# Kernel optimization log

Measured on AMD Instinct MI355X. Metric: run time of the kernel, lower is better.

## Reference

```python
import jax, jax.numpy as jnp
import numpy as np

DIM = 192
HEADS = 6
HD = DIM // HEADS            # 32
RES = (32, 64, 64)           # D, H, W
WS = (4, 4, 4)               # window size
NW_TOK = WS[0] * WS[1] * WS[2]   # 64 tokens per window
L = RES[0] * RES[1] * RES[2]     # 131072
HIDDEN = 4 * DIM
B = 2


def _rel_pos_index():
    # faithful to the torch buffer construction (3D branch)
    coords = np.stack(np.meshgrid(*[np.arange(w) for w in WS], indexing='ij'))  # (3, wd, wh, ww)
    cf = coords.reshape(3, -1)                     # (3, 64)
    rel = cf[:, :, None] - cf[:, None, :]          # (3, 64, 64)
    rel = rel.transpose(1, 2, 0).astype(np.int64)  # (64, 64, 3)
    for i in range(3):
        rel[:, :, i] += WS[i] - 1
    rel[:, :, 0] *= (2 * WS[1] - 1) * (2 * WS[2] - 1)
    rel[:, :, 1] *= 2 * WS[2] - 1
    return rel.sum(-1)                             # (64, 64)


def setup_inputs() -> dict:
    key = jax.random.key(0)
    ks = jax.random.split(key, 8)
    s = 0.02
    d = {}
    d['skip'] = jax.random.normal(ks[0], (B, L, DIM), jnp.float32)
    d['x_up'] = jax.random.normal(ks[1], (B, L, DIM), jnp.float32)
    # norms
    d['g1'] = jnp.ones((DIM,), jnp.float32); d['be1'] = jnp.zeros((DIM,), jnp.float32)
    d['g2'] = jnp.ones((DIM,), jnp.float32); d['be2'] = jnp.zeros((DIM,), jnp.float32)
    # attention params
    d['Wkv'] = jax.random.normal(ks[2], (DIM, 2 * DIM), jnp.float32) * s
    d['bkv'] = jnp.zeros((2 * DIM,), jnp.float32)
    d['Wproj'] = jax.random.normal(ks[3], (DIM, DIM), jnp.float32) * s
    d['bproj'] = jnp.zeros((DIM,), jnp.float32)
    d['bias_table'] = jax.random.normal(ks[4], ((2 * WS[0] - 1) * (2 * WS[1] - 1) * (2 * WS[2] - 1), HEADS), jnp.float32) * s
    d['rel_idx'] = jnp.asarray(_rel_pos_index(), jnp.int32)
    # MLP params
    d['W1'] = jax.random.normal(ks[5], (DIM, HIDDEN), jnp.float32) * s
    d['b1'] = jnp.zeros((HIDDEN,), jnp.float32)
    d['W2'] = jax.random.normal(ks[6], (HIDDEN, DIM), jnp.float32) * s
    d['b2'] = jnp.zeros((DIM,), jnp.float32)
    return d


def _ln(x, g, b):
    mu = x.mean(-1, keepdims=True)
    var = x.var(-1, keepdims=True)
    return (x - mu) * jax.lax.rsqrt(var + 1e-5) * g + b


def _win_part(x):
    # x: (B, D, H, W, C) -> (B*nW, 64, C)
    D, H, W = RES; wd, wh, ww = WS
    x = x.reshape(B, D // wd, wd, H // wh, wh, W // ww, ww, DIM)
    x = x.transpose(0, 1, 3, 5, 2, 4, 6, 7)
    return x.reshape(-1, NW_TOK, DIM)


def _win_rev(w):
    # (B*nW, 64, C) -> (B, L, C)
    D, H, W = RES; wd, wh, ww = WS
    x = w.reshape(B, D // wd, H // wh, W // ww, wd, wh, ww, DIM)
    x = x.transpose(0, 1, 4, 2, 5, 3, 6, 7)
    return x.reshape(B, L, DIM)


def reference(skip, x_up, g1, be1, g2, be2, Wkv, bkv, Wproj, bproj,
              bias_table, rel_idx, W1, b1, W2, b2):
    shortcut = skip
    s = _ln(skip, g1, be1).reshape(B, *RES, DIM)
    u = _ln(x_up, g1, be1).reshape(B, *RES, DIM)
    sw = _win_part(s)   # kv source: (Bw, 64, C)
    uw = _win_part(u)   # q source
    Bw = sw.shape[0]
    kv = (sw @ Wkv + bkv).reshape(Bw, NW_TOK, 2, HEADS, HD)
    k = kv[:, :, 0].transpose(0, 2, 1, 3)   # (Bw, h, 64, hd)
    v = kv[:, :, 1].transpose(0, 2, 1, 3)
    q = uw.reshape(Bw, NW_TOK, HEADS, HD).transpose(0, 2, 1, 3)
    scale = HD ** -0.5
    attn = jnp.einsum('bhqd,bhkd->bhqk', q * scale, k)
    bias = bias_table[rel_idx.reshape(-1)].reshape(NW_TOK, NW_TOK, HEADS).transpose(2, 0, 1)
    attn = jax.nn.softmax(attn + bias[None], axis=-1)
    o = jnp.einsum('bhqk,bhkd->bhqd', attn, v).transpose(0, 2, 1, 3).reshape(Bw, NW_TOK, DIM)
    o = o @ Wproj + bproj
    x = shortcut + _win_rev(o)
    h = _ln(x, g2, be2)
    h = jax.nn.gelu(h @ W1 + b1, approximate=False)
    return x + (h @ W2 + b2)
```

## Files before the change

kernel.cpp:

```cpp
#include <hip/hip_runtime.h>
#include <hip/hip_bf16.h>

typedef __hip_bfloat16 bf16;
typedef short s8v __attribute__((ext_vector_type(8)));
typedef float f32x4 __attribute__((ext_vector_type(4)));

__device__ __forceinline__ float b2f(bf16 v) { return __bfloat162float(v); }
__device__ __forceinline__ bf16 f2b(float v) { return __float2bfloat16(v); }

union H8 { bf16 h[8]; s8v v; uint2 u2[2]; };

__device__ __forceinline__ float gelu_f(float v) {
    float z = fabsf(v) * 0.70710678118654752f;
    float t = 1.f / (1.f + 0.3275911f * z);
    float poly = t * (0.254829592f + t * (-0.284496736f + t * (1.421413741f +
                 t * (-1.453152027f + t * 1.061405429f))));
    float erfz = 1.f - poly * __expf(-z * z);
    erfz = copysignf(erfz, v);
    return 0.5f * v * (1.f + erfz);
}

__device__ __forceinline__ void stage_frag(const bf16* __restrict__ img, bf16* lds,
                                           int nseg, int wv, int lane) {
    for (int seg = wv; seg < nseg; seg += 4) {
        __builtin_amdgcn_global_load_lds(
            (const __attribute__((address_space(1))) void*)(img + seg * 512 + (lane << 3)),
            (__attribute__((address_space(3))) void*)(lds + seg * 512),
            16, 0, 0);
    }
}

__global__ __launch_bounds__(256) void k_prep(
    const float* __restrict__ Wkv, const float* __restrict__ Wproj,
    const float* __restrict__ W1,  const float* __restrict__ W2,
    bf16* __restrict__ ws)
{
    int t = blockIdx.x * 256 + threadIdx.x;
    if (t >= 50688) return;
    int k, n, ld;
    const float* W;
    bf16* dst;
    if (t < 9216) {
        int c = t / 1152, r = t % 1152;
        int tile = r >> 6, lane = r & 63;
        int ks = tile / 3, nt = tile % 3;
        n = c * 48 + nt * 16 + (lane & 15);
        k = ks * 32 + (lane >> 4) * 8;
        W = Wkv; ld = 384; dst = ws + t * 8;
    } else if (t < 13824) {
        int t2 = t - 9216;
        int c = t2 / 1152, r = t2 % 1152;
        int tile = r >> 6, lane = r & 63;
        int ks = tile / 3, nt = tile % 3;
        n = c * 48 + nt * 16 + (lane & 15);
        k = ks * 32 + (lane >> 4) * 8;
        W = Wproj; ld = 192; dst = ws + 73728 + t2 * 8;
    } else {
        int t3 = t - 13824;
        int c = t3 / 1536, r = t3 % 1536;
        int half = r / 768, rr = r % 768;
        int tile = rr >> 6, lane = rr & 63;
        int lr = lane & 15, g = lane >> 4;
        if (half == 0) {
            int ks = tile >> 1, nt2 = tile & 1;
            n = c * 32 + nt2 * 16 + lr; k = ks * 32 + g * 8; W = W1; ld = 768;
        } else {
            n = tile * 16 + lr; k = c * 32 + g * 8; W = W2; ld = 192;
        }
        dst = ws + 110592 + t3 * 8;
    }
    #pragma unroll
    for (int e = 0; e < 8; ++e) dst[e] = f2b(W[(k + e) * ld + n]);
}

__global__ __launch_bounds__(256, 2) void k_attn(
    const float* __restrict__ skip, const float* __restrict__ xup,
    const float* __restrict__ g1,   const float* __restrict__ be1,
    const bf16*  __restrict__ imgKv,const float* __restrict__ bkv,
    const bf16*  __restrict__ imgPr,const float* __restrict__ bproj,
    const float* __restrict__ btab, const int*  __restrict__ relidx,
    float* __restrict__ xout)
{
    __shared__ __align__(16) bf16 sK[64 * 200];
    __shared__ __align__(16) char poolRaw[36864];
    __shared__ __align__(1024) bf16 sWt[9216];

    bf16* sVt = (bf16*)poolRaw;
    bf16* sP  = (bf16*)(poolRaw + 27648);
    bf16* sO  = (bf16*)poolRaw;
    float* sBt = (float*)sWt;

    const int tid = threadIdx.x;
    const int lane = tid & 63;
    const int wv = tid >> 6;
    const int g = lane >> 4;
    const int lr = lane & 15;
    const int w = blockIdx.x;
    const int b = w >> 11;
    const int widx = w & 2047;
    const int d0 = widx >> 8, h0 = (widx >> 4) & 15, w0 = widx & 15;

    #define GROW(t) (b * 131072 + (d0 * 4 + ((t) >> 4)) * 4096 + \
                     (h0 * 4 + (((t) >> 2) & 3)) * 64 + (w0 * 4 + ((t) & 3)))

    const int myrow = wv * 16 + lr;
    const int growA = GROW(myrow) * 192;
    float4 u4[12], s4[12];
    #pragma unroll
    for (int ks = 0; ks < 6; ++ks) {
        int k0 = 32 * ks + 8 * g;
        u4[2 * ks]     = *(const float4*)(xup  + growA + k0);
        u4[2 * ks + 1] = *(const float4*)(xup  + growA + k0 + 4);
        s4[2 * ks]     = *(const float4*)(skip + growA + k0);
        s4[2 * ks + 1] = *(const float4*)(skip + growA + k0 + 4);
    }
    float su = 0, squ = 0, ss = 0, sqs = 0;
    #pragma unroll
    for (int i = 0; i < 12; ++i) {
        const float* up = &u4[i].x;
        const float* sp = &s4[i].x;
        #pragma unroll
        for (int e = 0; e < 4; ++e) {
            su += up[e]; squ += up[e] * up[e];
            ss += sp[e]; sqs += sp[e] * sp[e];
        }
    }
    su += __shfl_xor(su, 16);  su += __shfl_xor(su, 32);
    squ += __shfl_xor(squ, 16); squ += __shfl_xor(squ, 32);
    ss += __shfl_xor(ss, 16);  ss += __shfl_xor(ss, 32);
    sqs += __shfl_xor(sqs, 16); sqs += __shfl_xor(sqs, 32);
    const float inv192 = 1.f / 192.f;
    float muU = su * inv192, vU = squ * inv192 - muU * muU;
    float muS = ss * inv192, vS = sqs * inv192 - muS * muS;
    float rU = rsqrtf(vU + 1e-5f), rS = rsqrtf(vS + 1e-5f);
    const float scale = 0.17677669529663687f;

    s8v qreg[6], sreg[6];
    #pragma unroll
    for (int ks = 0; ks < 6; ++ks) {
        H8 qa, sa;
        #pragma unroll
        for (int half = 0; half < 2; ++half) {
            const float* up = &u4[2 * ks + half].x;
            const float* sp = &s4[2 * ks + half].x;
            #pragma unroll
            for (int e = 0; e < 4; ++e) {
                int k = 32 * ks + 8 * g + 4 * half + e;
                float gg = g1[k], bb = be1[k];
                qa.h[4 * half + e] = f2b(((up[e] - muU) * rU * gg + bb) * scale);
                sa.h[4 * half + e] = f2b((sp[e] - muS) * rS * gg + bb);
            }
        }
        qreg[ks] = qa.v; sreg[ks] = sa.v;
    }

    for (int nc = 0; nc < 8; ++nc) {
        __syncthreads();
        stage_frag(imgKv + nc * 9216, sWt, 18, wv, lane);
        __syncthreads();

        f32x4 acc[3];
        #pragma unroll
        for (int nt = 0; nt < 3; ++nt) acc[nt] = (f32x4){0.f, 0.f, 0.f, 0.f};
        #pragma unroll
        for (int ks = 0; ks < 6; ++ks) {
            #pragma unroll
            for (int nt = 0; nt < 3; ++nt) {
                s8v bfr = *(const s8v*)(sWt + ((ks * 3 + nt) * 64 + lane) * 8);
                acc[nt] = __builtin_amdgcn_mfma_f32_16x16x32_bf16(sreg[ks], bfr, acc[nt], 0, 0, 0);
            }
        }
        if (nc < 4) {
            #pragma unroll
            for (int nt = 0; nt < 3; ++nt) {
                int c = nc * 48 + nt * 16 + lr;
                float bias = bkv[c];
                #pragma unroll
                for (int e = 0; e < 4; ++e)
                    sK[(wv * 16 + 4 * g + e) * 200 + c] = f2b(acc[nt][e] + bias);
            }
        } else {
            #pragma unroll
            for (int nt = 0; nt < 3; ++nt) {
                int c = nc * 48 + nt * 16 + lr;
                float bias = bkv[c];
                int d = c - 192;
                H8 t4;
                #pragma unroll
                for (int e = 0; e < 4; ++e) t4.h[e] = f2b(acc[nt][e] + bias);
                *(uint2*)(sVt + d * 72 + wv * 16 + 4 * g) = t4.u2[0];
            }
        }
    }
    __syncthreads();

    for (int i = tid; i < 2058; i += 256) sBt[i] = btab[i];
    int bidx[4][4];
    #pragma unroll
    for (int nt = 0; nt < 4; ++nt)
        #pragma unroll
        for (int e = 0; e < 4; ++e)
            bidx[nt][e] = relidx[(wv * 16 + lr) * 64 + nt * 16 + 4 * g + e] * 6;
    __syncthreads();

    f32x4 accOT[6][2];
    #pragma unroll
    for (int h = 0; h < 6; ++h)
        #pragma unroll
        for (int nt = 0; nt < 2; ++nt) accOT[h][nt] = (f32x4){0.f, 0.f, 0.f, 0.f};

    #pragma unroll
    for (int h = 0; h < 6; ++h) {
        f32x4 s[4];
        #pragma unroll
        for (int nt = 0; nt < 4; ++nt) {
            s8v kf = *(const s8v*)(sK + (nt * 16 + lr) * 200 + h * 32 + 8 * g);
            s[nt] = __builtin_amdgcn_mfma_f32_16x16x32_bf16(kf, qreg[h],
                        (f32x4){0.f, 0.f, 0.f, 0.f}, 0, 0, 0);
        }
        #pragma unroll
        for (int nt = 0; nt < 4; ++nt)
            #pragma unroll
            for (int e = 0; e < 4; ++e)
                s[nt][e] += sBt[bidx[nt][e] + h];
        float mx = -1e30f;
        #pragma unroll
        for (int nt = 0; nt < 4; ++nt)
            #pragma unroll
            for (int e = 0; e < 4; ++e) mx = fmaxf(mx, s[nt][e]);
        mx = fmaxf(mx, __shfl_xor(mx, 16));
        mx = fmaxf(mx, __shfl_xor(mx, 32));
        float sm = 0;
        #pragma unroll
        for (int nt = 0; nt < 4; ++nt)
            #pragma unroll
            for (int e = 0; e < 4; ++e) { s[nt][e] = __expf(s[nt][e] - mx); sm += s[nt][e]; }
        sm += __shfl_xor(sm, 16);
        sm += __shfl_xor(sm, 32);
        float iv = 1.f / sm;
        #pragma unroll
        for (int nt = 0; nt < 4; ++nt) {
            H8 pk;
            #pragma unroll
            for (int e = 0; e < 4; ++e) pk.h[e] = f2b(s[nt][e] * iv);
            *(uint2*)(sP + (wv * 16 + lr) * 72 + nt * 16 + 4 * g) = pk.u2[0];
        }
        s8v aP0 = *(const s8v*)(sP + (wv * 16 + lr) * 72 + 8 * g);
        s8v aP1 = *(const s8v*)(sP + (wv * 16 + lr) * 72 + 32 + 8 * g);
        #pragma unroll
        for (int nt = 0; nt < 2; ++nt) {
            const bf16* vb = sVt + (h * 32 + nt * 16 + lr) * 72;
            s8v v0 = *(const s8v*)(vb + 8 * g);
            s8v v1 = *(const s8v*)(vb + 32 + 8 * g);
            accOT[h][nt] = __builtin_amdgcn_mfma_f32_16x16x32_bf16(v0, aP0, accOT[h][nt], 0, 0, 0);
            accOT[h][nt] = __builtin_amdgcn_mfma_f32_16x16x32_bf16(v1, aP1, accOT[h][nt], 0, 0, 0);
        }
    }

    __syncthreads();
    #pragma unroll
    for (int h = 0; h < 6; ++h)
        #pragma unroll
        for (int nt = 0; nt < 2; ++nt) {
            H8 pk;
            #pragma unroll
            for (int e = 0; e < 4; ++e) pk.h[e] = f2b(accOT[h][nt][e]);
            *(uint2*)(sO + (wv * 16 + lr) * 200 + h * 32 + nt * 16 + 4 * g) = pk.u2[0];
        }
    s8v aO[6];
    #pragma unroll
    for (int ks = 0; ks < 6; ++ks)
        aO[ks] = *(const s8v*)(sO + (wv * 16 + lr) * 200 + 32 * ks + 8 * g);

    int gq[4];
    #pragma unroll
    for (int e = 0; e < 4; ++e) gq[e] = GROW(wv * 16 + 4 * g + e) * 192;

    for (int nc = 0; nc < 4; ++nc) {
        __syncthreads();
        stage_frag(imgPr + nc * 9216, sWt, 18, wv, lane);
        __syncthreads();

        f32x4 acc[3];
        #pragma unroll
        for (int nt = 0; nt < 3; ++nt) acc[nt] = (f32x4){0.f, 0.f, 0.f, 0.f};
        #pragma unroll
        for (int ks = 0; ks < 6; ++ks) {
            #pragma unroll
            for (int nt = 0; nt < 3; ++nt) {
                s8v bfr = *(const s8v*)(sWt + ((ks * 3 + nt) * 64 + lane) * 8);
                acc[nt] = __builtin_amdgcn_mfma_f32_16x16x32_bf16(aO[ks], bfr, acc[nt], 0, 0, 0);
            }
        }
        #pragma unroll
        for (int nt = 0; nt < 3; ++nt) {
            int c = nc * 48 + nt * 16 + lr;
            float bp = bproj[c];
            #pragma unroll
            for (int e = 0; e < 4; ++e) {
                int go = gq[e] + c;
                xout[go] = acc[nt][e] + bp + skip[go];
            }
        }
    }
    #undef GROW
}

__global__ __launch_bounds__(256, 2) void k_mlp(
    float* __restrict__ xio,
    const float* __restrict__ g2, const float* __restrict__ be2,
    const bf16*  __restrict__ imgMlp,
    const float* __restrict__ b1, const float* __restrict__ b2)
{
    __shared__ __align__(1024) bf16 sW[2][12288];
    __shared__ __align__(16) bf16 sH[128 * 40];

    const int tid = threadIdx.x;
    const int lane = tid & 63;
    const int wv = tid >> 6;
    const int g = lane >> 4;
    const int lr = lane & 15;
    const int rowbase = blockIdx.x * 128;

    stage_frag(imgMlp, sW[0], 24, wv, lane);

    s8v xreg[2][6];
    #pragma unroll
    for (int mi = 0; mi < 2; ++mi) {
        const int row = rowbase + wv * 16 + mi * 64 + lr;
        float4 xa[12];
        #pragma unroll
        for (int ks = 0; ks < 6; ++ks) {
            int k0 = 32 * ks + 8 * g;
            xa[2 * ks]     = *(const float4*)(xio + row * 192 + k0);
            xa[2 * ks + 1] = *(const float4*)(xio + row * 192 + k0 + 4);
        }
        float s = 0, sq = 0;
        #pragma unroll
        for (int i = 0; i < 12; ++i) {
            const float* p = &xa[i].x;
            #pragma unroll
            for (int e = 0; e < 4; ++e) { s += p[e]; sq += p[e] * p[e]; }
        }
        s += __shfl_xor(s, 16);  s += __shfl_xor(s, 32);
        sq += __shfl_xor(sq, 16); sq += __shfl_xor(sq, 32);
        float mu = s * (1.f / 192.f), var = sq * (1.f / 192.f) - mu * mu;
        float rs = rsqrtf(var + 1e-5f);
        #pragma unroll
        for (int ks = 0; ks < 6; ++ks) {
            H8 xa8;
            #pragma unroll
            for (int half = 0; half < 2; ++half) {
                int k0 = 32 * ks + 8 * g + 4 * half;
                float4 gg = *(const float4*)(g2 + k0);
                float4 be = *(const float4*)(be2 + k0);
                const float* p = &xa[2 * ks + half].x;
                const float* gp = &gg.x;
                const float* bp = &be.x;
                #pragma unroll
                for (int e = 0; e < 4; ++e)
                    xa8.h[4 * half + e] = f2b((p[e] - mu) * rs * gp[e] + bp[e]);
            }
            xreg[mi][ks] = xa8.v;
        }
    }

    f32x4 accC[2][12];
    #pragma unroll
    for (int mi = 0; mi < 2; ++mi)
        #pragma unroll
        for (int nt = 0; nt < 12; ++nt) accC[mi][nt] = (f32x4){0.f, 0.f, 0.f, 0.f};

    for (int ch = 0; ch < 24; ++ch) {
        const int c = ch & 1;
        __syncthreads();
        if (ch < 23) stage_frag(imgMlp + (ch + 1) * 12288, sW[c ^ 1], 24, wv, lane);
        const bf16* wc = sW[c];

        f32x4 accHT[2][2];
        #pragma unroll
        for (int mi = 0; mi < 2; ++mi)
            #pragma unroll
            for (int nt = 0; nt < 2; ++nt) accHT[mi][nt] = (f32x4){0.f, 0.f, 0.f, 0.f};
        #pragma unroll
        for (int ks = 0; ks < 6; ++ks) {
            s8v w0 = *(const s8v*)(wc + ((ks * 2 + 0) * 64 + lane) * 8);
            s8v w1 = *(const s8v*)(wc + ((ks * 2 + 1) * 64 + lane) * 8);
            accHT[0][0] = __builtin_amdgcn_mfma_f32_16x16x32_bf16(w0, xreg[0][ks], accHT[0][0], 0, 0, 0);
            accHT[0][1] = __builtin_amdgcn_mfma_f32_16x16x32_bf16(w1, xreg[0][ks], accHT[0][1], 0, 0, 0);
            accHT[1][0] = __builtin_amdgcn_mfma_f32_16x16x32_bf16(w0, xreg[1][ks], accHT[1][0], 0, 0, 0);
            accHT[1][1] = __builtin_amdgcn_mfma_f32_16x16x32_bf16(w1, xreg[1][ks], accHT[1][1], 0, 0, 0);
        }

        #pragma unroll
        for (int mi = 0; mi < 2; ++mi)
            #pragma unroll
            for (int nt2 = 0; nt2 < 2; ++nt2) {
                float4 b1v = *(const float4*)(b1 + ch * 32 + nt2 * 16 + 4 * g);
                const float* bp = &b1v.x;
                H8 pk;
                #pragma unroll
                for (int e = 0; e < 4; ++e)
                    pk.h[e] = f2b(gelu_f(accHT[mi][nt2][e] + bp[e]));
                *(uint2*)(sH + (wv * 16 + mi * 64 + lr) * 40 + nt2 * 16 + 4 * g) = pk.u2[0];
            }

        s8v aH0 = *(const s8v*)(sH + (wv * 16 + lr) * 40 + g * 8);
        s8v aH1 = *(const s8v*)(sH + (wv * 16 + 64 + lr) * 40 + g * 8);
        #pragma unroll
        for (int nt = 0; nt < 12; ++nt) {
            s8v bW = *(const s8v*)(wc + 6144 + (nt * 64 + lane) * 8);
            accC[0][nt] = __builtin_amdgcn_mfma_f32_16x16x32_bf16(aH0, bW, accC[0][nt], 0, 0, 0);
            accC[1][nt] = __builtin_amdgcn_mfma_f32_16x16x32_bf16(aH1, bW, accC[1][nt], 0, 0, 0);
        }
    }

    #pragma unroll
    for (int mi = 0; mi < 2; ++mi)
        #pragma unroll
        for (int nt = 0; nt < 12; ++nt) {
            int col = nt * 16 + lr;
            float bb = b2[col];
            #pragma unroll
            for (int e = 0; e < 4; ++e) {
                int row = rowbase + wv * 16 + mi * 64 + g * 4 + e;
                float* p = xio + row * 192 + col;
                *p = accC[mi][nt][e] + bb + *p;
            }
        }
}

extern "C" void kernel_launch(void* const* d_in, const int* in_sizes, int n_in,
                              void* d_out, int out_size, void* d_ws, size_t ws_size,
                              hipStream_t stream) {
    const float* skip   = (const float*)d_in[0];
    const float* xup    = (const float*)d_in[1];
    const float* g1     = (const float*)d_in[2];
    const float* be1    = (const float*)d_in[3];
    const float* g2     = (const float*)d_in[4];
    const float* be2    = (const float*)d_in[5];
    const float* Wkv    = (const float*)d_in[6];
    const float* bkv    = (const float*)d_in[7];
    const float* Wproj  = (const float*)d_in[8];
    const float* bproj  = (const float*)d_in[9];
    const float* btab   = (const float*)d_in[10];
    const int*  relidx  = (const int*)d_in[11];
    const float* W1     = (const float*)d_in[12];
    const float* b1     = (const float*)d_in[13];
    const float* W2     = (const float*)d_in[14];
    const float* b2     = (const float*)d_in[15];
    float* xio = (float*)d_out;
    bf16* ws = (bf16*)d_ws;

    k_prep<<<198, 256, 0, stream>>>(Wkv, Wproj, W1, W2, ws);
    k_attn<<<4096, 256, 0, stream>>>(skip, xup, g1, be1, ws, bkv,
                                     ws + 73728, bproj, btab, relidx, xio);
    k_mlp<<<2048, 256, 0, stream>>>(xio, g2, be2, ws + 110592, b1, b2);
}
```

Measured before the change: 586.6 us.

## Read attention weights from global, single-buffer MLP weights, use tanh GELU

In the attention kernel, weight fragments for the KV and projection GEMMs are now loaded directly from global memory instead of being staged in LDS, removing per-chunk barriers. The bias table gets its own LDS array and is loaded earlier. The MLP kernel's double-buffered weight staging becomes a single buffer with a barrier after each load, halving that LDS footprint but removing prefetch overlap. The erf-based GELU is replaced with the tanh approximation expressed as a sigmoid, which is cheaper but slightly changes numerics.

```diff
diff --git a/kernel.cpp b/kernel.cpp
--- a/kernel.cpp
+++ b/kernel.cpp
@@ -10,14 +10,12 @@
 
 union H8 { bf16 h[8]; s8v v; uint2 u2[2]; };
 
-__device__ __forceinline__ float gelu_f(float v) {
-    float z = fabsf(v) * 0.70710678118654752f;
-    float t = 1.f / (1.f + 0.3275911f * z);
-    float poly = t * (0.254829592f + t * (-0.284496736f + t * (1.421413741f +
-                 t * (-1.453152027f + t * 1.061405429f))));
-    float erfz = 1.f - poly * __expf(-z * z);
-    erfz = copysignf(erfz, v);
-    return 0.5f * v * (1.f + erfz);
+__device__ __forceinline__ float gelu_f(float x) {
+    float x2 = x * x;
+    float t = fmaf(x2, 0.044715f, 1.0f);
+    float u = x * 1.5957691216057308f * t;
+    float e = __expf(-u);
+    return x / (1.0f + e);
 }
 
 __device__ __forceinline__ void stage_frag(const bf16* __restrict__ img, bf16* lds,
@@ -83,12 +81,11 @@
 {
     __shared__ __align__(16) bf16 sK[64 * 200];
     __shared__ __align__(16) char poolRaw[36864];
-    __shared__ __align__(1024) bf16 sWt[9216];
+    __shared__ __align__(16) float sBt[2058];
 
     bf16* sVt = (bf16*)poolRaw;
     bf16* sP  = (bf16*)(poolRaw + 27648);
     bf16* sO  = (bf16*)poolRaw;
-    float* sBt = (float*)sWt;
 
     const int tid = threadIdx.x;
     const int lane = tid & 63;
@@ -154,11 +151,10 @@
         qreg[ks] = qa.v; sreg[ks] = sa.v;
     }
 
+    for (int i = tid; i < 2058; i += 256) sBt[i] = btab[i];
+
     for (int nc = 0; nc < 8; ++nc) {
-        __syncthreads();
-        stage_frag(imgKv + nc * 9216, sWt, 18, wv, lane);
-        __syncthreads();
-
+        const bf16* img = imgKv + nc * 9216;
         f32x4 acc[3];
         #pragma unroll
         for (int nt = 0; nt < 3; ++nt) acc[nt] = (f32x4){0.f, 0.f, 0.f, 0.f};
@@ -166,7 +162,7 @@
         for (int ks = 0; ks < 6; ++ks) {
             #pragma unroll
             for (int nt = 0; nt < 3; ++nt) {
-                s8v bfr = *(const s8v*)(sWt + ((ks * 3 + nt) * 64 + lane) * 8);
+                s8v bfr = *(const s8v*)(img + ((ks * 3 + nt) * 64 + lane) * 8);
                 acc[nt] = __builtin_amdgcn_mfma_f32_16x16x32_bf16(sreg[ks], bfr, acc[nt], 0, 0, 0);
             }
         }
@@ -192,15 +188,14 @@
             }
         }
     }
-    __syncthreads();
-
-    for (int i = tid; i < 2058; i += 256) sBt[i] = btab[i];
+
     int bidx[4][4];
     #pragma unroll
     for (int nt = 0; nt < 4; ++nt)
         #pragma unroll
         for (int e = 0; e < 4; ++e)
             bidx[nt][e] = relidx[(wv * 16 + lr) * 64 + nt * 16 + 4 * g + e] * 6;
+
     __syncthreads();
 
     f32x4 accOT[6][2];
@@ -258,6 +253,7 @@
     }
 
     __syncthreads();
+
     #pragma unroll
     for (int h = 0; h < 6; ++h)
         #pragma unroll
@@ -277,10 +273,7 @@
     for (int e = 0; e < 4; ++e) gq[e] = GROW(wv * 16 + 4 * g + e) * 192;
 
     for (int nc = 0; nc < 4; ++nc) {
-        __syncthreads();
-        stage_frag(imgPr + nc * 9216, sWt, 18, wv, lane);
-        __syncthreads();
-
+        const bf16* img = imgPr + nc * 9216;
         f32x4 acc[3];
         #pragma unroll
         for (int nt = 0; nt < 3; ++nt) acc[nt] = (f32x4){0.f, 0.f, 0.f, 0.f};
@@ -288,7 +281,7 @@
         for (int ks = 0; ks < 6; ++ks) {
             #pragma unroll
             for (int nt = 0; nt < 3; ++nt) {
-                s8v bfr = *(const s8v*)(sWt + ((ks * 3 + nt) * 64 + lane) * 8);
+                s8v bfr = *(const s8v*)(img + ((ks * 3 + nt) * 64 + lane) * 8);
                 acc[nt] = __builtin_amdgcn_mfma_f32_16x16x32_bf16(aO[ks], bfr, acc[nt], 0, 0, 0);
             }
         }
@@ -312,7 +305,7 @@
     const bf16*  __restrict__ imgMlp,
     const float* __restrict__ b1, const float* __restrict__ b2)
 {
-    __shared__ __align__(1024) bf16 sW[2][12288];
+    __shared__ __align__(1024) bf16 sW[12288];
     __shared__ __align__(16) bf16 sH[128 * 40];
 
     const int tid = threadIdx.x;
@@ -321,8 +314,6 @@
     const int g = lane >> 4;
     const int lr = lane & 15;
     const int rowbase = blockIdx.x * 128;
-
-    stage_frag(imgMlp, sW[0], 24, wv, lane);
 
     s8v xreg[2][6];
     #pragma unroll
@@ -372,10 +363,9 @@
         for (int nt = 0; nt < 12; ++nt) accC[mi][nt] = (f32x4){0.f, 0.f, 0.f, 0.f};
 
     for (int ch = 0; ch < 24; ++ch) {
-        const int c = ch & 1;
         __syncthreads();
-        if (ch < 23) stage_frag(imgMlp + (ch + 1) * 12288, sW[c ^ 1], 24, wv, lane);
-        const bf16* wc = sW[c];
+        stage_frag(imgMlp + ch * 12288, sW, 24, wv, lane);
+        __syncthreads();
 
         f32x4 accHT[2][2];
         #pragma unroll
@@ -384,8 +374,8 @@
             for (int nt = 0; nt < 2; ++nt) accHT[mi][nt] = (f32x4){0.f, 0.f, 0.f, 0.f};
         #pragma unroll
         for (int ks = 0; ks < 6; ++ks) {
-            s8v w0 = *(const s8v*)(wc + ((ks * 2 + 0) * 64 + lane) * 8);
-            s8v w1 = *(const s8v*)(wc + ((ks * 2 + 1) * 64 + lane) * 8);
+            s8v w0 = *(const s8v*)(sW + ((ks * 2 + 0) * 64 + lane) * 8);
+            s8v w1 = *(const s8v*)(sW + ((ks * 2 + 1) * 64 + lane) * 8);
             accHT[0][0] = __builtin_amdgcn_mfma_f32_16x16x32_bf16(w0, xreg[0][ks], accHT[0][0], 0, 0, 0);
             accHT[0][1] = __builtin_amdgcn_mfma_f32_16x16x32_bf16(w1, xreg[0][ks], accHT[0][1], 0, 0, 0);
             accHT[1][0] = __builtin_amdgcn_mfma_f32_16x16x32_bf16(w0, xreg[1][ks], accHT[1][0], 0, 0, 0);
@@ -409,7 +399,7 @@
         s8v aH1 = *(const s8v*)(sH + (wv * 16 + 64 + lr) * 40 + g * 8);
         #pragma unroll
         for (int nt = 0; nt < 12; ++nt) {
-            s8v bW = *(const s8v*)(wc + 6144 + (nt * 64 + lane) * 8);
+            s8v bW = *(const s8v*)(sW + 6144 + (nt * 64 + lane) * 8);
             accC[0][nt] = __builtin_amdgcn_mfma_f32_16x16x32_bf16(aH0, bW, accC[0][nt], 0, 0, 0);
             accC[1][nt] = __builtin_amdgcn_mfma_f32_16x16x32_bf16(aH1, bW, accC[1][nt], 0, 0, 0);
         }
```

Result: no change. 585.7 us (-0.2%).
